# Optimization experiments

Measured on AMD Instinct MI355X. Metric: run time of the kernel, lower is better.

The kernel has to match this reference:

```python
import jax, jax.numpy as jnp
import numpy as np

C, RES = 32, 512
PLANE_DIMIDS = [(0, 1), (0, 2), (1, 2)]  # combinations(range(3), 2)


def _bilinear_sample(plane, gx, gy):
    """grid_sample(mode='bilinear', align_corners=True) for one plane.
    plane: (C, H, W); gx, gy: (B,) normalized coords in [-1, 1]
    (gx indexes W, gy indexes H, matching torch grid_sample convention).
    Returns (B, C)."""
    _, H, W = plane.shape
    ix = (gx + 1.0) * 0.5 * (W - 1)  # align_corners=True mapping
    iy = (gy + 1.0) * 0.5 * (H - 1)
    x0f = jnp.floor(ix)
    y0f = jnp.floor(iy)
    wx = ix - x0f  # fractional weights
    wy = iy - y0f
    x0 = jnp.clip(x0f.astype(jnp.int32), 0, W - 1)
    x1 = jnp.clip(x0 + 1, 0, W - 1)
    y0 = jnp.clip(y0f.astype(jnp.int32), 0, H - 1)
    y1 = jnp.clip(y0 + 1, 0, H - 1)
    # gathers: (C, B) each
    v00 = plane[:, y0, x0]
    v01 = plane[:, y0, x1]
    v10 = plane[:, y1, x0]
    v11 = plane[:, y1, x1]
    out = (v00 * ((1 - wx) * (1 - wy)) + v01 * (wx * (1 - wy))
           + v10 * ((1 - wx) * wy) + v11 * (wx * wy))
    return out.T  # (B, C)


def setup_inputs() -> dict:
    key = jax.random.key(0)
    kx, k0, k1, k2 = jax.random.split(key, 4)
    x = jax.random.uniform(kx, (2000000, 3), dtype=jnp.float32)  # in [0,1) subset of [-1,1]
    # planes ~ U(0.01, 0.25) per torch.nn.init.uniform_(a=0.01, b=0.25); shape (C, H, W)
    def mk(k):
        return jax.random.uniform(k, (C, RES, RES), dtype=jnp.float32,
                                  minval=0.01, maxval=0.25)
    return {"x": x, "p0": mk(k0), "p1": mk(k1), "p2": mk(k2)}


def reference(x, p0, p1, p2):
    feats = None
    for plane, (da, db) in zip((p0, p1, p2), PLANE_DIMIDS):
        f = _bilinear_sample(plane, x[:, da], x[:, db])  # (B, C)
        feats = f if feats is None else feats * f
    return feats  # (B, C) == original feats.T
```

## Files before the change

### kernel.cpp

```cpp
#include <hip/hip_runtime.h>
#include <hip/hip_fp16.h>

#define RES 512
#define NCH 32
#define HW (RES * RES)
#define PLANE_H_ELEMS (NCH * HW)
#define NBUCKETS 4096
#define NGRP 128

typedef float vfloat4 __attribute__((ext_vector_type(4)));

__device__ __forceinline__ unsigned spread3(unsigned x) {
    x &= 0x3FF;
    x = (x | (x << 16)) & 0x030000FF;
    x = (x | (x <<  8)) & 0x0300F00F;
    x = (x | (x <<  4)) & 0x030C30C3;
    x = (x | (x <<  2)) & 0x09249249;
    return x;
}
__device__ __forceinline__ unsigned bucket_of(float c0, float c1, float c2) {
    int bx = min(max((int)(c0 * 16.f), 0), 15);
    int by = min(max((int)(c1 * 16.f), 0), 15);
    int bz = min(max((int)(c2 * 16.f), 0), 15);
    return spread3(bx) | (spread3(by) << 1) | (spread3(bz) << 2);
}

__global__ __launch_bounds__(512) void prep_kernel(
    const float* __restrict__ p0, const float* __restrict__ p1,
    const float* __restrict__ p2, __half2* __restrict__ dst_all,
    const float* __restrict__ x, int npts, unsigned* __restrict__ cnt)
{
    __shared__ char smem[17408];
    int blk = blockIdx.x;
    int t   = threadIdx.x;

    if (blk < NGRP) {
        unsigned* lh = (unsigned*)smem;
        for (int i = t; i < NBUCKETS; i += 512) lh[i] = 0;
        __syncthreads();
        int seg = (npts + NGRP - 1) / NGRP;
        int start = blk * seg;
        int end = min(npts, start + seg);
        for (int i = start + t; i < end; i += 512) {
            float c0 = x[3 * i + 0], c1 = x[3 * i + 1], c2 = x[3 * i + 2];
            atomicAdd(&lh[bucket_of(c0, c1, c2)], 1u);
        }
        __syncthreads();
        unsigned* dst = cnt + (size_t)blk * NBUCKETS;
        for (int i = t; i < NBUCKETS; i += 512) dst[i] = lh[i];
        return;
    }

    float* lds = (float*)smem;
    int tp   = blk - NGRP;
    int sub  = t >> 8;
    int tt   = t & 255;
    int tile = tp * 2 + sub;
    int plane = tile >> 12;
    int rem   = tile & 4095;
    int y     = rem >> 3;
    int xt    = (rem & 7) << 6;
    const float* src = (plane == 0) ? p0 : (plane == 1) ? p1 : p2;
    __half2* dst = dst_all + (size_t)plane * (PLANE_H_ELEMS / 2);
    float* myl = lds + sub * 2112;

    #pragma unroll
    for (int k = 0; k < 8; ++k) {
        int idx = tt + (k << 8);
        int c   = idx >> 6;
        int xi  = idx & 63;
        myl[xi * 33 + c] = src[(size_t)c * HW + (size_t)y * RES + xt + xi];
    }
    __syncthreads();
    #pragma unroll
    for (int k = 0; k < 4; ++k) {
        int idx = tt + (k << 8);
        int xi  = idx >> 4;
        int cp  = idx & 15;
        __half2 h = __halves2half2(__float2half_rn(myl[xi * 33 + 2 * cp]),
                                   __float2half_rn(myl[xi * 33 + 2 * cp + 1]));
        dst[((size_t)(y * RES + xt + xi)) * 16 + cp] = h;
    }
}

__global__ __launch_bounds__(256) void group_prefix_kernel(
    const unsigned* __restrict__ cnt, unsigned* __restrict__ offs,
    unsigned* __restrict__ total)
{
    int bucket = blockIdx.x * 256 + threadIdx.x;
    unsigned run = 0;
    for (int g = 0; g < NGRP; ++g) {
        unsigned v = cnt[(size_t)g * NBUCKETS + bucket];
        offs[(size_t)g * NBUCKETS + bucket] = run;
        run += v;
    }
    total[bucket] = run;
}

__global__ __launch_bounds__(1024) void scan_kernel(
    const unsigned* __restrict__ hist, unsigned* __restrict__ offs)
{
    __shared__ unsigned sd[1024];
    int t = threadIdx.x;
    unsigned h0 = hist[4 * t + 0], h1 = hist[4 * t + 1];
    unsigned h2 = hist[4 * t + 2], h3 = hist[4 * t + 3];
    sd[t] = h0 + h1 + h2 + h3;
    __syncthreads();
    for (int d = 1; d < 1024; d <<= 1) {
        unsigned v = (t >= d) ? sd[t - d] : 0u;
        __syncthreads();
        sd[t] += v;
        __syncthreads();
    }
    unsigned excl = (t > 0) ? sd[t - 1] : 0u;
    offs[4 * t + 0] = excl;
    offs[4 * t + 1] = excl + h0;
    offs[4 * t + 2] = excl + h0 + h1;
    offs[4 * t + 3] = excl + h0 + h1 + h2;
}

__global__ __launch_bounds__(512) void scatter_ranked_kernel(
    const float* __restrict__ x, int npts, const unsigned* __restrict__ base,
    const unsigned* __restrict__ offs, float4* __restrict__ sorted)
{
    __shared__ unsigned posb[NBUCKETS];
    __shared__ unsigned lcnt[NBUCKETS];
    int g = blockIdx.x, t = threadIdx.x;
    for (int i = t; i < NBUCKETS; i += 512) {
        posb[i] = base[i] + offs[(size_t)g * NBUCKETS + i];
        lcnt[i] = 0;
    }
    __syncthreads();
    int seg = (npts + NGRP - 1) / NGRP;
    int start = g * seg;
    int end = min(npts, start + seg);
    for (int i = start + t; i < end; i += 512) {
        float c0 = x[3 * i + 0], c1 = x[3 * i + 1], c2 = x[3 * i + 2];
        unsigned b = bucket_of(c0, c1, c2);
        unsigned r = atomicAdd(&lcnt[b], 1u);
        sorted[posb[b] + r] = make_float4(c0, c1, c2, __int_as_float(i));
    }
}

__device__ __forceinline__ float2 dec2(unsigned u) {
    return __half22float2(__builtin_bit_cast(__half2, u));
}
__device__ __forceinline__ void bilerp2(float2& acc, unsigned c00, unsigned c01,
                                        unsigned c10, unsigned c11,
                                        float w00, float w01, float w10, float w11) {
    float2 a = dec2(c00), b = dec2(c01), c = dec2(c10), d = dec2(c11);
    float f0 = fmaf(a.x, w00, fmaf(b.x, w01, fmaf(c.x, w10, d.x * w11)));
    float f1 = fmaf(a.y, w00, fmaf(b.y, w01, fmaf(c.y, w10, d.y * w11)));
    acc.x *= f0; acc.y *= f1;
}

__global__ __launch_bounds__(256, 4) void sample_sorted_u4(
    const float4* __restrict__ sorted, const __half* __restrict__ planes,
    float* __restrict__ out, int npts, int nb_q, int nb_r)
{
    int bid = blockIdx.x;
    int xcd = bid & 7;
    int j   = bid >> 3;
    int chunk = (xcd < nb_r ? xcd * (nb_q + 1) : nb_r * (nb_q + 1) + (xcd - nb_r) * nb_q) + j;

    int s = chunk * 64 + (threadIdx.x >> 2);
    int q = threadIdx.x & 3;
    if (s >= npts) return;

    float4 p = sorted[s];
    int b = __float_as_int(p.w);

    const float gxs[3] = { p.x, p.x, p.y };
    const float gys[3] = { p.y, p.z, p.z };

    const __half* base[3];
    float w00[3], w01[3], w10[3], w11[3];
    #pragma unroll
    for (int pl = 0; pl < 3; ++pl) {
        float ix = fmaf(gxs[pl], 255.5f, 255.5f);
        float iy = fmaf(gys[pl], 255.5f, 255.5f);
        float xf = floorf(ix), yf = floorf(iy);
        float wx = ix - xf,  wy = iy - yf;
        int x0 = min(max((int)xf, 0), RES - 2);
        int y0 = min(max((int)yf, 0), RES - 2);
        base[pl] = planes + (size_t)pl * PLANE_H_ELEMS
                 + (size_t)(y0 * RES + x0) * NCH + q * 8;
        float omx = 1.f - wx, omy = 1.f - wy;
        w00[pl] = omx * omy; w01[pl] = wx * omy;
        w10[pl] = omx * wy;  w11[pl] = wx * wy;
    }

    uint4 u00[3], u01[3], u10[3], u11[3];
    #pragma unroll
    for (int pl = 0; pl < 3; ++pl) {
        u00[pl] = *(const uint4*)(base[pl]);
        u01[pl] = *(const uint4*)(base[pl] + NCH);
        u10[pl] = *(const uint4*)(base[pl] + RES * NCH);
        u11[pl] = *(const uint4*)(base[pl] + RES * NCH + NCH);
    }

    float2 acc0 = {1.f, 1.f}, acc1 = {1.f, 1.f}, acc2 = {1.f, 1.f}, acc3 = {1.f, 1.f};
    #pragma unroll
    for (int pl = 0; pl < 3; ++pl) {
        bilerp2(acc0, u00[pl].x, u01[pl].x, u10[pl].x, u11[pl].x,
                w00[pl], w01[pl], w10[pl], w11[pl]);
        bilerp2(acc1, u00[pl].y, u01[pl].y, u10[pl].y, u11[pl].y,
                w00[pl], w01[pl], w10[pl], w11[pl]);
        bilerp2(acc2, u00[pl].z, u01[pl].z, u10[pl].z, u11[pl].z,
                w00[pl], w01[pl], w10[pl], w11[pl]);
        bilerp2(acc3, u00[pl].w, u01[pl].w, u10[pl].w, u11[pl].w,
                w00[pl], w01[pl], w10[pl], w11[pl]);
    }

    float* op = out + (size_t)b * NCH + q * 8;
    vfloat4 lo = { acc0.x, acc0.y, acc1.x, acc1.y };
    vfloat4 hi = { acc2.x, acc2.y, acc3.x, acc3.y };
    __builtin_nontemporal_store(lo, (vfloat4*)op);
    __builtin_nontemporal_store(hi, (vfloat4*)(op + 4));
}

__global__ __launch_bounds__(256) void triplane_sample_chw(
    const float* __restrict__ x, const float* __restrict__ p0,
    const float* __restrict__ p1, const float* __restrict__ p2,
    float* __restrict__ out, int npts)
{
    int gid = blockIdx.x * 256 + threadIdx.x;
    int b = gid >> 5;
    int c = gid & 31;
    if (b >= npts) return;

    float c0 = x[b * 3 + 0], c1 = x[b * 3 + 1], c2 = x[b * 3 + 2];
    const float gxs[3] = { c0, c0, c1 };
    const float gys[3] = { c1, c2, c2 };
    const float* planes[3] = { p0, p1, p2 };

    float acc = 1.f;
    #pragma unroll
    for (int pl = 0; pl < 3; ++pl) {
        float ix = fmaf(gxs[pl], 255.5f, 255.5f);
        float iy = fmaf(gys[pl], 255.5f, 255.5f);
        float xf = floorf(ix), yf = floorf(iy);
        float wx = ix - xf,  wy = iy - yf;
        int x0 = min(max((int)xf, 0), RES - 2);
        int y0 = min(max((int)yf, 0), RES - 2);

        const float* base = planes[pl] + (size_t)c * HW + (size_t)y0 * RES + x0;
        float v00 = base[0], v01 = base[1], v10 = base[RES], v11 = base[RES + 1];

        float omx = 1.f - wx, omy = 1.f - wy;
        acc *= fmaf(v00, omx * omy, fmaf(v01, wx * omy,
               fmaf(v10, omx * wy, v11 * (wx * wy))));
    }
    out[(size_t)b * NCH + c] = acc;
}

extern "C" void kernel_launch(void* const* d_in, const int* in_sizes, int n_in,
                              void* d_out, int out_size, void* d_ws, size_t ws_size,
                              hipStream_t stream) {
    const float* x  = (const float*)d_in[0];
    const float* p0 = (const float*)d_in[1];
    const float* p1 = (const float*)d_in[2];
    const float* p2 = (const float*)d_in[3];
    float* out = (float*)d_out;
    int npts = in_sizes[0] / 3;

    size_t planes_bytes = (size_t)3 * PLANE_H_ELEMS * sizeof(__half);
    size_t sorted_bytes = (size_t)npts * sizeof(float4);
    size_t cnt_bytes    = (size_t)NGRP * NBUCKETS * sizeof(unsigned);
    size_t offs_bytes   = cnt_bytes;
    size_t tot_bytes    = NBUCKETS * sizeof(unsigned);
    size_t need = planes_bytes + sorted_bytes + cnt_bytes + offs_bytes + 2 * tot_bytes;

    if (ws_size >= need) {
        char* ws = (char*)d_ws;
        __half*   planes_h = (__half*)ws;
        float4*   sorted   = (float4*)(ws + planes_bytes);
        unsigned* cnt      = (unsigned*)(ws + planes_bytes + sorted_bytes);
        unsigned* offs     = cnt + (size_t)NGRP * NBUCKETS;
        unsigned* total    = offs + (size_t)NGRP * NBUCKETS;
        unsigned* base     = total + NBUCKETS;

        prep_kernel<<<NGRP + 6144, 512, 0, stream>>>(p0, p1, p2,
                                                     (__half2*)planes_h, x, npts, cnt);
        group_prefix_kernel<<<NBUCKETS / 256, 256, 0, stream>>>(cnt, offs, total);
        scan_kernel<<<1, 1024, 0, stream>>>(total, base);
        scatter_ranked_kernel<<<NGRP, 512, 0, stream>>>(x, npts, base, offs, sorted);

        int nchunks = (npts + 63) / 64;
        int nb_q = nchunks / 8, nb_r = nchunks & 7;
        sample_sorted_u4<<<nchunks, 256, 0, stream>>>(sorted, planes_h, out, npts, nb_q, nb_r);
    } else {
        long long nthreads = (long long)npts * 32;
        int blocks = (int)((nthreads + 255) / 256);
        triplane_sample_chw<<<blocks, 256, 0, stream>>>(x, p0, p1, p2, out, npts);
    }
}
```

Before: 168.6 us.

## Fold bucket scan into scatter kernel and double histogram groups

Removes the separate single-block scan kernel launch. Each scatter block now recomputes the exclusive prefix over the 4096 bucket totals in shared memory before scattering. The number of point groups goes from 128 to 256, which gives the histogram and scatter stages more parallelism but makes the group prefix loop twice as long. The per-group prefix loop is also unrolled. The cost is redundant scan work in every scatter block and larger count/offset arrays.

```diff
diff --git a/kernel.cpp b/kernel.cpp
--- a/kernel.cpp
+++ b/kernel.cpp
@@ -6,7 +6,7 @@
 #define HW (RES * RES)
 #define PLANE_H_ELEMS (NCH * HW)
 #define NBUCKETS 4096
-#define NGRP 128
+#define NGRP 256
 
 typedef float vfloat4 __attribute__((ext_vector_type(4)));
 
@@ -89,6 +89,7 @@
 {
     int bucket = blockIdx.x * 256 + threadIdx.x;
     unsigned run = 0;
+    #pragma unroll 4
     for (int g = 0; g < NGRP; ++g) {
         unsigned v = cnt[(size_t)g * NBUCKETS + bucket];
         offs[(size_t)g * NBUCKETS + bucket] = run;
@@ -97,40 +98,37 @@
     total[bucket] = run;
 }
 
-__global__ __launch_bounds__(1024) void scan_kernel(
-    const unsigned* __restrict__ hist, unsigned* __restrict__ offs)
-{
-    __shared__ unsigned sd[1024];
-    int t = threadIdx.x;
-    unsigned h0 = hist[4 * t + 0], h1 = hist[4 * t + 1];
-    unsigned h2 = hist[4 * t + 2], h3 = hist[4 * t + 3];
-    sd[t] = h0 + h1 + h2 + h3;
-    __syncthreads();
-    for (int d = 1; d < 1024; d <<= 1) {
-        unsigned v = (t >= d) ? sd[t - d] : 0u;
-        __syncthreads();
-        sd[t] += v;
-        __syncthreads();
-    }
-    unsigned excl = (t > 0) ? sd[t - 1] : 0u;
-    offs[4 * t + 0] = excl;
-    offs[4 * t + 1] = excl + h0;
-    offs[4 * t + 2] = excl + h0 + h1;
-    offs[4 * t + 3] = excl + h0 + h1 + h2;
-}
-
 __global__ __launch_bounds__(512) void scatter_ranked_kernel(
-    const float* __restrict__ x, int npts, const unsigned* __restrict__ base,
+    const float* __restrict__ x, int npts, const unsigned* __restrict__ total,
     const unsigned* __restrict__ offs, float4* __restrict__ sorted)
 {
     __shared__ unsigned posb[NBUCKETS];
     __shared__ unsigned lcnt[NBUCKETS];
+    __shared__ unsigned partial[512];
     int g = blockIdx.x, t = threadIdx.x;
-    for (int i = t; i < NBUCKETS; i += 512) {
-        posb[i] = base[i] + offs[(size_t)g * NBUCKETS + i];
-        lcnt[i] = 0;
-    }
+
+    unsigned v[8], s = 0;
+    #pragma unroll
+    for (int k = 0; k < 8; ++k) { v[k] = total[8 * t + k]; s += v[k]; }
+    partial[t] = s;
     __syncthreads();
+    for (int d = 1; d < 512; d <<= 1) {
+        unsigned u = (t >= d) ? partial[t - d] : 0u;
+        __syncthreads();
+        partial[t] += u;
+        __syncthreads();
+    }
+    unsigned excl = (t > 0) ? partial[t - 1] : 0u;
+    unsigned run = excl;
+    #pragma unroll
+    for (int k = 0; k < 8; ++k) {
+        int b = 8 * t + k;
+        posb[b] = run + offs[(size_t)g * NBUCKETS + b];
+        lcnt[b] = 0;
+        run += v[k];
+    }
+    __syncthreads();
+
     int seg = (npts + NGRP - 1) / NGRP;
     int start = g * seg;
     int end = min(npts, start + seg);
@@ -269,7 +267,7 @@
     size_t cnt_bytes    = (size_t)NGRP * NBUCKETS * sizeof(unsigned);
     size_t offs_bytes   = cnt_bytes;
     size_t tot_bytes    = NBUCKETS * sizeof(unsigned);
-    size_t need = planes_bytes + sorted_bytes + cnt_bytes + offs_bytes + 2 * tot_bytes;
+    size_t need = planes_bytes + sorted_bytes + cnt_bytes + offs_bytes + tot_bytes;
 
     if (ws_size >= need) {
         char* ws = (char*)d_ws;
@@ -278,13 +276,11 @@
         unsigned* cnt      = (unsigned*)(ws + planes_bytes + sorted_bytes);
         unsigned* offs     = cnt + (size_t)NGRP * NBUCKETS;
         unsigned* total    = offs + (size_t)NGRP * NBUCKETS;
-        unsigned* base     = total + NBUCKETS;
 
         prep_kernel<<<NGRP + 6144, 512, 0, stream>>>(p0, p1, p2,
                                                      (__half2*)planes_h, x, npts, cnt);
         group_prefix_kernel<<<NBUCKETS / 256, 256, 0, stream>>>(cnt, offs, total);
-        scan_kernel<<<1, 1024, 0, stream>>>(total, base);
-        scatter_ranked_kernel<<<NGRP, 512, 0, stream>>>(x, npts, base, offs, sorted);
+        scatter_ranked_kernel<<<NGRP, 512, 0, stream>>>(x, npts, total, offs, sorted);
 
         int nchunks = (npts + 63) / 64;
         int nb_q = nchunks / 8, nb_r = nchunks & 7;
```

After: 177.0 us. 1.05x slower.
